# Kernel tuning notes

Hardware: AMD Instinct MI355X
Metric: run time of the kernel (lower is better)

Reference implementation:

```python
import jax, jax.numpy as jnp
import numpy as np

# MORR all-pass ring parameters (MORRConfig_20um defaults: attenuation / self-coupling)
A_MORR = 0.8578
R_MORR = 0.8578
KS = 3       # kernel_size
MB = 8       # miniblock (circulant block size)
BN_EPS = 1e-5


def mrr_roundtrip_phase_to_tr(phi):
    # through-port transmission of an all-pass microring vs roundtrip phase
    c = jnp.cos(phi)
    num = A_MORR * A_MORR - 2.0 * A_MORR * R_MORR * c + R_MORR * R_MORR
    den = 1.0 - 2.0 * A_MORR * R_MORR * c + (A_MORR * R_MORR) ** 2
    return num / den


def setup_inputs() -> dict:
    key = jax.random.key(0)
    k1, k2 = jax.random.split(key, 2)
    B, C, H, W = 64, 64, 32, 32
    outC = 64
    q = (C * KS * KS + MB - 1) // MB   # grid_dim_x = 72
    p = (outC + MB - 1) // MB          # grid_dim_y = 8
    x = jax.random.normal(k1, (B, C, H, W), jnp.float32)
    weight = jax.random.normal(k2, (p, q, MB), jnp.float32) * 0.05  # circulant eigen-vectors per block
    gamma = jnp.ones((outC,), jnp.float32)   # BatchNorm2d weight
    beta = jnp.zeros((outC,), jnp.float32)   # BatchNorm2d bias
    return {"x": x, "weight": weight, "gamma": gamma, "beta": beta}


def reference(x, weight, gamma, beta):
    B, C, H, W = x.shape
    p, q, mb = weight.shape
    outC = gamma.shape[0]
    Ho, Wo = H, W  # stride=1, padding=1, ks=3
    L = Ho * Wo
    # im2col (torch F.unfold ordering: C major, then kh, kw)
    xp = jnp.pad(x, ((0, 0), (0, 0), (1, 1), (1, 1)))
    cols = jnp.stack([xp[:, :, i:i + Ho, j:j + Wo]
                      for i in range(KS) for j in range(KS)], axis=2)  # [B,C,9,Ho,Wo]
    cols = cols.reshape(B, C * KS * KS, L).transpose(0, 2, 1)          # [B,L,C*k*k]
    assert C * KS * KS == q * mb, "patch dim must pad to q*mb"
    s = cols.reshape(B, L, q, mb)
    s = s * s  # optical intensity (power) fed into the MORR
    # block-circulant weight: Wc[p,q,i,j] = weight[p,q,(i-j) mod mb]
    i_idx = jnp.arange(mb)
    idx = (i_idx[:, None] - i_idx[None, :]) % mb
    Wc = weight[:, :, idx]                                             # [p,q,mb,mb]
    # accumulated roundtrip phase per output node
    phase = jnp.einsum('blqj,pqij->blpi', s, Wc)                       # [B,L,p,mb]
    tr = mrr_roundtrip_phase_to_tr(phase)
    out = tr.reshape(B, L, p * mb)[:, :, :outC]                        # truncate to out_channel
    out = out.transpose(0, 2, 1).reshape(B, outC, Ho, Wo)
    # BatchNorm2d (training mode: batch statistics) + Hardtanh(-1, 1)
    mean = out.mean(axis=(0, 2, 3), keepdims=True)
    var = out.var(axis=(0, 2, 3), keepdims=True)
    y = (out - mean) * jax.lax.rsqrt(var + BN_EPS)
    y = y * gamma[None, :, None, None] + beta[None, :, None, None]
    return jnp.clip(y, -1.0, 1.0)
```

## Files before the change

### kernel.cpp

```cpp
#include <hip/hip_runtime.h>


#define A_MORR 0.8578f
#define R_MORR 0.8578f
#define TR_C1 (A_MORR * A_MORR + R_MORR * R_MORR)
#define TR_C2 (-2.0f * A_MORR * R_MORR)
#define TR_C3 (1.0f + (A_MORR * R_MORR) * (A_MORR * R_MORR))
#define BN_EPS 1e-5f

#define NPIX 65536
#define X2_LO 26112
#define SMEM_BYTES 52224
#define NBLK 512

typedef __attribute__((ext_vector_type(8))) short bf16x8;
typedef __attribute__((ext_vector_type(16))) float f32x16;

__device__ __forceinline__ void bf16split(float s, unsigned short& h, unsigned short& l) {
    union { float f; unsigned u; } cv; cv.f = s;
    unsigned r = (cv.u + 0x7fffu + ((cv.u >> 16) & 1u)) & 0xffff0000u;
    h = (unsigned short)(r >> 16);
    union { unsigned u; float f; } hv; hv.u = r;
    float lo = s - hv.f;
    cv.f = lo;
    unsigned r2 = cv.u + 0x7fffu + ((cv.u >> 16) & 1u);
    l = (unsigned short)(r2 >> 16);
}

__global__ __launch_bounds__(256) void prep_kernel(const float* __restrict__ w,
                                                   char* __restrict__ wfrag) {
    int gtid = blockIdx.x * 256 + threadIdx.x;
    if (gtid < 36864) {
        int j    = gtid & 7;
        int lane = (gtid >> 3) & 63;
        int okm  = gtid >> 9;
        int mt   = okm & 1;
        int ks   = (okm >> 1) & 3;
        int off  = okm >> 3;
        int oc   = mt * 32 + (lane & 31);
        int c    = ks * 16 + (lane >> 5) * 8 + j;
        int kg   = c * 9 + off;
        float val = w[(oc >> 3) * 576 + (kg >> 3) * 8 + ((oc - kg) & 7)];
        unsigned short h, l;
        bf16split(val, h, l);
        ((unsigned short*)(wfrag + okm * 2048))[lane * 8 + j] = h;
        ((unsigned short*)(wfrag + okm * 2048 + 1024))[lane * 8 + j] = l;
    }
}

__global__ __launch_bounds__(512, 2) void conv_kernel(const float* __restrict__ x,
                                                      const char* __restrict__ wfrag,
                                                      float* __restrict__ out,
                                                      float* __restrict__ partials) {
    const int rt  = blockIdx.x;
    const int b   = blockIdx.y;
    const int bid = b * 8 + rt;
    const int tid = threadIdx.x;

    __shared__ __align__(16) char smem[SMEM_BYTES];

    if (tid < 192) {
        int prec = tid & 1;
        int g    = (tid >> 1) & 7;
        int rc   = tid >> 4;
        int r    = rc >> 1;
        int c    = (rc & 1) ? 33 : 0;
        *(uint4*)(smem + prec * X2_LO + ((r * 34 + c) << 7) + (g << 4)) = uint4{0, 0, 0, 0};
    }

    {
        const int rh  = tid & 1;
        const int co  = (tid >> 1) & 7;
        const int chp = tid >> 4;
        const float* xb = x + (size_t)(b * 64 + 2 * chp) * 1024;
#pragma unroll
        for (int r3 = 0; r3 < 3; ++r3) {
            int rr = rh * 3 + r3;
            int gr = rt * 4 - 1 + rr;
            float4 a0 = {0.f, 0.f, 0.f, 0.f}, a1 = {0.f, 0.f, 0.f, 0.f};
            if (gr >= 0 && gr < 32) {
                const float* rp = xb + gr * 32 + co * 4;
                a0 = *(const float4*)rp;
                a1 = *(const float4*)(rp + 1024);
            }
            float s0[4] = {a0.x * a0.x, a0.y * a0.y, a0.z * a0.z, a0.w * a0.w};
            float s1[4] = {a1.x * a1.x, a1.y * a1.y, a1.z * a1.z, a1.w * a1.w};
#pragma unroll
            for (int i = 0; i < 4; ++i) {
                unsigned short h0, l0, h1, l1;
                bf16split(s0[i], h0, l0);
                bf16split(s1[i], h1, l1);
                int c    = 1 + co * 4 + i;
                int base = ((rr * 34 + c) << 7) + (((chp >> 2) ^ (c & 7)) << 4)
                         + ((chp & 3) << 2);
                *(unsigned*)(smem + base)         = (unsigned)h0 | ((unsigned)h1 << 16);
                *(unsigned*)(smem + X2_LO + base) = (unsigned)l0 | ((unsigned)l1 << 16);
            }
        }
    }
    __syncthreads();

    const int lane = tid & 63;
    const int wv   = tid >> 6;
    const int wmt  = wv & 1;
    const int kh   = (wv >> 1) & 1;
    const int py   = wv >> 2;
    const int col  = lane & 31;
    const int hs   = lane >> 5;
    const int rowb = py * 2;

    f32x16 acc0, acc1;
#pragma unroll
    for (int i = 0; i < 16; ++i) { acc0[i] = 0.f; acc1[i] = 0.f; }

    const char* wbase = wfrag + wmt * 2048 + (size_t)lane * 16;

#pragma unroll
    for (int dj = 0; dj < 3; ++dj) {
        const int c  = col + dj;
        const int c7 = c & 7;
#pragma unroll
        for (int ksi = 0; ksi < 2; ++ksi) {
            const int ks = kh * 2 + ksi;
            const int g  = ((ks * 2 + hs) ^ c7) << 4;
            bf16x8 bh[4], bl[4];
#pragma unroll
            for (int rr = 0; rr < 4; ++rr) {
                const char* sp = smem + (((rowb + rr) * 34 + c) << 7) + g;
                bh[rr] = *(const bf16x8*)sp;
                bl[rr] = *(const bf16x8*)(sp + X2_LO);
            }
#pragma unroll
            for (int di = 0; di < 3; ++di) {
                const char* wp = wbase + (di * 3 + dj) * 16384 + ks * 4096;
                bf16x8 ah = *(const bf16x8*)wp;
                bf16x8 al = *(const bf16x8*)(wp + 1024);
                acc0 = __builtin_amdgcn_mfma_f32_32x32x16_bf16(ah, bh[di],     acc0, 0, 0, 0);
                acc1 = __builtin_amdgcn_mfma_f32_32x32x16_bf16(ah, bh[di + 1], acc1, 0, 0, 0);
                acc0 = __builtin_amdgcn_mfma_f32_32x32x16_bf16(ah, bl[di],     acc0, 0, 0, 0);
                acc1 = __builtin_amdgcn_mfma_f32_32x32x16_bf16(ah, bl[di + 1], acc1, 0, 0, 0);
                acc0 = __builtin_amdgcn_mfma_f32_32x32x16_bf16(al, bh[di],     acc0, 0, 0, 0);
                acc1 = __builtin_amdgcn_mfma_f32_32x32x16_bf16(al, bh[di + 1], acc1, 0, 0, 0);
            }
        }
    }

    float* mergef = (float*)smem;
    __syncthreads();
    {
        const int slot = (wmt * 2 + py) * 2;
        if (kh == 1) {
#pragma unroll
            for (int r = 0; r < 16; ++r) {
                mergef[((slot + 0) * 16 + r) * 64 + lane] = acc0[r];
                mergef[((slot + 1) * 16 + r) * 64 + lane] = acc1[r];
            }
        }
        __syncthreads();
        if (kh == 0) {
#pragma unroll
            for (int r = 0; r < 16; ++r) {
                float p0 = acc0[r] + mergef[((slot + 0) * 16 + r) * 64 + lane];
                float p1 = acc1[r] + mergef[((slot + 1) * 16 + r) * 64 + lane];
                float c0 = __cosf(p0);
                float c1 = __cosf(p1);
                acc0[r] = fmaf(TR_C2, c0, TR_C1) / fmaf(TR_C2, c0, TR_C3);
                acc1[r] = fmaf(TR_C2, c1, TR_C1) / fmaf(TR_C2, c1, TR_C3);
            }
        }
    }
    __syncthreads();

    float* red1 = mergef;
    float* red2 = red1 + 64 * 66;
    if (kh == 0) {
#pragma unroll
        for (int r = 0; r < 16; ++r) {
            int ocl  = (r & 3) + 8 * (r >> 2) + 4 * hs;
            float t0 = acc0[r], t1 = acc1[r];
            int ri = (wmt * 32 + ocl) * 66 + py * 32 + col;
            red1[ri] = t0 + t1;
            red2[ri] = t0 * t0 + t1 * t1;
        }
    }
    __syncthreads();
    if (tid < 64) {
        float s1 = 0.f, s2 = 0.f;
#pragma unroll
        for (int q = 0; q < 64; ++q) {
            s1 += red1[tid * 66 + q];
            s2 += red2[tid * 66 + q];
        }
        partials[(size_t)tid * NBLK + bid]        = s1;
        partials[(size_t)(64 + tid) * NBLK + bid] = s2;
    }

    if (kh == 0) {
        const size_t outbase = ((size_t)b * 64 + wmt * 32) * 1024 + rt * 128;
#pragma unroll
        for (int r = 0; r < 16; ++r) {
            int ocl  = (r & 3) + 8 * (r >> 2) + 4 * hs;
            size_t o = outbase + (size_t)ocl * 1024 + py * 64 + col;
            out[o]      = acc0[r];
            out[o + 32] = acc1[r];
        }
    }
}

__global__ __launch_bounds__(512) void stats_kernel(const float* __restrict__ partials,
                                                    const float* __restrict__ gamma,
                                                    const float* __restrict__ beta,
                                                    float* __restrict__ ss) {
    const int c   = blockIdx.x;
    const int tid = threadIdx.x;
    __shared__ float r1[512], r2[512];
    r1[tid] = partials[(size_t)c * NBLK + tid];
    r2[tid] = partials[(size_t)(64 + c) * NBLK + tid];
    __syncthreads();
#pragma unroll
    for (int s = 256; s > 0; s >>= 1) {
        if (tid < s) {
            r1[tid] += r1[tid + s];
            r2[tid] += r2[tid + s];
        }
        __syncthreads();
    }
    if (tid == 0) {
        const float invN = 1.0f / (float)NPIX;
        float mean = r1[0] * invN;
        float var  = r2[0] * invN - mean * mean;
        float sc   = gamma[c] * rsqrtf(var + BN_EPS);
        ss[c]      = sc;
        ss[64 + c] = beta[c] - mean * sc;
    }
}

__global__ __launch_bounds__(256) void norm_kernel(float* __restrict__ out,
                                                   const float* __restrict__ ss) {
    int i = blockIdx.x * 256 + threadIdx.x;
    float4 v = ((float4*)out)[i];
    int oc = (i >> 8) & 63;
    float sc = ss[oc];
    float sh = ss[64 + oc];
    v.x = fminf(1.0f, fmaxf(-1.0f, fmaf(v.x, sc, sh)));
    v.y = fminf(1.0f, fmaxf(-1.0f, fmaf(v.y, sc, sh)));
    v.z = fminf(1.0f, fmaxf(-1.0f, fmaf(v.z, sc, sh)));
    v.w = fminf(1.0f, fmaxf(-1.0f, fmaf(v.w, sc, sh)));
    ((float4*)out)[i] = v;
}

extern "C" void kernel_launch(void* const* d_in, const int* in_sizes, int n_in,
                              void* d_out, int out_size, void* d_ws, size_t ws_size,
                              hipStream_t stream) {
    const float* x     = (const float*)d_in[0];
    const float* w     = (const float*)d_in[1];
    const float* gamma = (const float*)d_in[2];
    const float* beta  = (const float*)d_in[3];
    float* out = (float*)d_out;

    char*  wfrag    = (char*)d_ws;
    float* partials = (float*)((char*)d_ws + 147456);
    float* ss       = partials + 128 * NBLK;

    hipLaunchKernelGGL(prep_kernel, dim3(144), dim3(256), 0, stream, w, wfrag);
    hipLaunchKernelGGL(conv_kernel, dim3(8, 64), dim3(512), 0, stream, x, wfrag, out, partials);
    hipLaunchKernelGGL(stats_kernel, dim3(64), dim3(512), 0, stream, partials, gamma, beta, ss);
    hipLaunchKernelGGL(norm_kernel, dim3(4096), dim3(256), 0, stream, out, ss);
}
```

Before: 42.00 us.

## Split K across four waves, register-cache weights, fuse epilogue with stats

Changes the wave decomposition from a 2x2 split over row pairs and K halves to a four-way K split, with each wave computing all four output rows. This lets each wave reuse B fragments across four accumulators, and the wave's nine weight fragments are preloaded into registers before the staging phase. Partial sums are merged through LDS in a chained sequence of five barriers. The transmission epilogue is fused with the output stores and the per-thread stat accumulation. Register pressure rises (four accumulators plus 18 weight vectors), and the serialized merge adds barriers and leaves only one wave in each M-tile half doing the epilogue.

After: 45.91 us. 9.3% more time.

```diff
diff --git a/kernel.cpp b/kernel.cpp
--- a/kernel.cpp
+++ b/kernel.cpp
@@ -57,7 +57,24 @@
     const int bid = b * 8 + rt;
     const int tid = threadIdx.x;
 
+    const int lane = tid & 63;
+    const int wv   = tid >> 6;
+    const int wmt  = wv & 1;
+    const int kq   = wv >> 1;
+    const int col  = lane & 31;
+    const int hs   = lane >> 5;
+
     __shared__ __align__(16) char smem[SMEM_BYTES];
+
+    bf16x8 wh[9], wl[9];
+    {
+        const char* wbase = wfrag + (size_t)wmt * 2048 + kq * 4096 + lane * 16;
+#pragma unroll
+        for (int t = 0; t < 9; ++t) {
+            wh[t] = *(const bf16x8*)(wbase + t * 16384);
+            wl[t] = *(const bf16x8*)(wbase + t * 16384 + 1024);
+        }
+    }
 
     if (tid < 192) {
         int prec = tid & 1;
@@ -100,110 +117,106 @@
     }
     __syncthreads();
 
-    const int lane = tid & 63;
-    const int wv   = tid >> 6;
-    const int wmt  = wv & 1;
-    const int kh   = (wv >> 1) & 1;
-    const int py   = wv >> 2;
-    const int col  = lane & 31;
-    const int hs   = lane >> 5;
-    const int rowb = py * 2;
-
-    f32x16 acc0, acc1;
-#pragma unroll
-    for (int i = 0; i < 16; ++i) { acc0[i] = 0.f; acc1[i] = 0.f; }
-
-    const char* wbase = wfrag + wmt * 2048 + (size_t)lane * 16;
+    f32x16 acc0, acc1, acc2, acc3;
+#pragma unroll
+    for (int i = 0; i < 16; ++i) { acc0[i] = 0.f; acc1[i] = 0.f; acc2[i] = 0.f; acc3[i] = 0.f; }
 
 #pragma unroll
     for (int dj = 0; dj < 3; ++dj) {
         const int c  = col + dj;
-        const int c7 = c & 7;
-#pragma unroll
-        for (int ksi = 0; ksi < 2; ++ksi) {
-            const int ks = kh * 2 + ksi;
-            const int g  = ((ks * 2 + hs) ^ c7) << 4;
-            bf16x8 bh[4], bl[4];
-#pragma unroll
-            for (int rr = 0; rr < 4; ++rr) {
-                const char* sp = smem + (((rowb + rr) * 34 + c) << 7) + g;
-                bh[rr] = *(const bf16x8*)sp;
-                bl[rr] = *(const bf16x8*)(sp + X2_LO);
-            }
-#pragma unroll
-            for (int di = 0; di < 3; ++di) {
-                const char* wp = wbase + (di * 3 + dj) * 16384 + ks * 4096;
-                bf16x8 ah = *(const bf16x8*)wp;
-                bf16x8 al = *(const bf16x8*)(wp + 1024);
-                acc0 = __builtin_amdgcn_mfma_f32_32x32x16_bf16(ah, bh[di],     acc0, 0, 0, 0);
-                acc1 = __builtin_amdgcn_mfma_f32_32x32x16_bf16(ah, bh[di + 1], acc1, 0, 0, 0);
-                acc0 = __builtin_amdgcn_mfma_f32_32x32x16_bf16(ah, bl[di],     acc0, 0, 0, 0);
-                acc1 = __builtin_amdgcn_mfma_f32_32x32x16_bf16(ah, bl[di + 1], acc1, 0, 0, 0);
-                acc0 = __builtin_amdgcn_mfma_f32_32x32x16_bf16(al, bh[di],     acc0, 0, 0, 0);
-                acc1 = __builtin_amdgcn_mfma_f32_32x32x16_bf16(al, bh[di + 1], acc1, 0, 0, 0);
-            }
-        }
-    }
-
-    float* mergef = (float*)smem;
-    __syncthreads();
-    {
-        const int slot = (wmt * 2 + py) * 2;
-        if (kh == 1) {
-#pragma unroll
-            for (int r = 0; r < 16; ++r) {
-                mergef[((slot + 0) * 16 + r) * 64 + lane] = acc0[r];
-                mergef[((slot + 1) * 16 + r) * 64 + lane] = acc1[r];
-            }
-        }
-        __syncthreads();
-        if (kh == 0) {
-#pragma unroll
-            for (int r = 0; r < 16; ++r) {
-                float p0 = acc0[r] + mergef[((slot + 0) * 16 + r) * 64 + lane];
-                float p1 = acc1[r] + mergef[((slot + 1) * 16 + r) * 64 + lane];
-                float c0 = __cosf(p0);
-                float c1 = __cosf(p1);
-                acc0[r] = fmaf(TR_C2, c0, TR_C1) / fmaf(TR_C2, c0, TR_C3);
-                acc1[r] = fmaf(TR_C2, c1, TR_C1) / fmaf(TR_C2, c1, TR_C3);
-            }
-        }
-    }
-    __syncthreads();
-
-    float* red1 = mergef;
-    float* red2 = red1 + 64 * 66;
-    if (kh == 0) {
-#pragma unroll
-        for (int r = 0; r < 16; ++r) {
-            int ocl  = (r & 3) + 8 * (r >> 2) + 4 * hs;
-            float t0 = acc0[r], t1 = acc1[r];
-            int ri = (wmt * 32 + ocl) * 66 + py * 32 + col;
-            red1[ri] = t0 + t1;
-            red2[ri] = t0 * t0 + t1 * t1;
+        const int g  = (((kq * 2 + hs) ^ (c & 7)) << 4);
+        bf16x8 bh[6], bl[6];
+#pragma unroll
+        for (int rr = 0; rr < 6; ++rr) {
+            const char* sp = smem + ((rr * 34 + c) << 7) + g;
+            bh[rr] = *(const bf16x8*)sp;
+            bl[rr] = *(const bf16x8*)(sp + X2_LO);
+        }
+#pragma unroll
+        for (int di = 0; di < 3; ++di) {
+            const bf16x8 ah = wh[di * 3 + dj];
+            const bf16x8 al = wl[di * 3 + dj];
+            acc0 = __builtin_amdgcn_mfma_f32_32x32x16_bf16(ah, bh[di + 0], acc0, 0, 0, 0);
+            acc1 = __builtin_amdgcn_mfma_f32_32x32x16_bf16(ah, bh[di + 1], acc1, 0, 0, 0);
+            acc2 = __builtin_amdgcn_mfma_f32_32x32x16_bf16(ah, bh[di + 2], acc2, 0, 0, 0);
+            acc3 = __builtin_amdgcn_mfma_f32_32x32x16_bf16(ah, bh[di + 3], acc3, 0, 0, 0);
+            acc0 = __builtin_amdgcn_mfma_f32_32x32x16_bf16(ah, bl[di + 0], acc0, 0, 0, 0);
+            acc1 = __builtin_amdgcn_mfma_f32_32x32x16_bf16(ah, bl[di + 1], acc1, 0, 0, 0);
+            acc2 = __builtin_amdgcn_mfma_f32_32x32x16_bf16(ah, bl[di + 2], acc2, 0, 0, 0);
+            acc3 = __builtin_amdgcn_mfma_f32_32x32x16_bf16(ah, bl[di + 3], acc3, 0, 0, 0);
+            acc0 = __builtin_amdgcn_mfma_f32_32x32x16_bf16(al, bh[di + 0], acc0, 0, 0, 0);
+            acc1 = __builtin_amdgcn_mfma_f32_32x32x16_bf16(al, bh[di + 1], acc1, 0, 0, 0);
+            acc2 = __builtin_amdgcn_mfma_f32_32x32x16_bf16(al, bh[di + 2], acc2, 0, 0, 0);
+            acc3 = __builtin_amdgcn_mfma_f32_32x32x16_bf16(al, bh[di + 3], acc3, 0, 0, 0);
+        }
+    }
+
+    float* mg = (float*)smem;
+#define SLOT_W() do {                                                          \
+    _Pragma("unroll") for (int j = 0; j < 16; ++j) {                           \
+        mg[((wmt * 4 + 0) * 16 + j) * 64 + lane] = acc0[j];                    \
+        mg[((wmt * 4 + 1) * 16 + j) * 64 + lane] = acc1[j];                    \
+        mg[((wmt * 4 + 2) * 16 + j) * 64 + lane] = acc2[j];                    \
+        mg[((wmt * 4 + 3) * 16 + j) * 64 + lane] = acc3[j];                    \
+    } } while (0)
+#define SLOT_A() do {                                                          \
+    _Pragma("unroll") for (int j = 0; j < 16; ++j) {                           \
+        acc0[j] += mg[((wmt * 4 + 0) * 16 + j) * 64 + lane];                   \
+        acc1[j] += mg[((wmt * 4 + 1) * 16 + j) * 64 + lane];                   \
+        acc2[j] += mg[((wmt * 4 + 2) * 16 + j) * 64 + lane];                   \
+        acc3[j] += mg[((wmt * 4 + 3) * 16 + j) * 64 + lane];                   \
+    } } while (0)
+
+    __syncthreads();
+    if (kq == 3) SLOT_W();
+    __syncthreads();
+    if (kq == 1) SLOT_A();
+    __syncthreads();
+    if (kq == 2) SLOT_W();
+    __syncthreads();
+    if (kq == 0) SLOT_A();
+    __syncthreads();
+    if (kq == 1) SLOT_W();
+    __syncthreads();
+
+    float* red1 = (float*)(smem + 32768);
+    float* red2 = red1 + 64 * 33;
+
+    if (kq == 0) {
+        SLOT_A();
+        float ts1[16], ts2[16];
+#pragma unroll
+        for (int j = 0; j < 16; ++j) { ts1[j] = 0.f; ts2[j] = 0.f; }
+        const size_t obase = ((size_t)b * 64 + wmt * 32) * 1024 + rt * 128;
+#define ROW_EPI(R, ACC) do {                                                   \
+    _Pragma("unroll") for (int j = 0; j < 16; ++j) {                           \
+        float cp = __cosf(ACC[j]);                                             \
+        float t  = fmaf(TR_C2, cp, TR_C1) / fmaf(TR_C2, cp, TR_C3);            \
+        int ocl  = (j & 3) + 8 * (j >> 2) + 4 * hs;                            \
+        out[obase + (size_t)ocl * 1024 + (R) * 32 + col] = t;                  \
+        ts1[j] += t; ts2[j] += t * t;                                          \
+    } } while (0)
+        ROW_EPI(0, acc0);
+        ROW_EPI(1, acc1);
+        ROW_EPI(2, acc2);
+        ROW_EPI(3, acc3);
+#pragma unroll
+        for (int j = 0; j < 16; ++j) {
+            int ocl = (j & 3) + 8 * (j >> 2) + 4 * hs;
+            red1[(wmt * 32 + ocl) * 33 + col] = ts1[j];
+            red2[(wmt * 32 + ocl) * 33 + col] = ts2[j];
         }
     }
     __syncthreads();
     if (tid < 64) {
         float s1 = 0.f, s2 = 0.f;
 #pragma unroll
-        for (int q = 0; q < 64; ++q) {
-            s1 += red1[tid * 66 + q];
-            s2 += red2[tid * 66 + q];
+        for (int q = 0; q < 32; ++q) {
+            s1 += red1[tid * 33 + q];
+            s2 += red2[tid * 33 + q];
         }
         partials[(size_t)tid * NBLK + bid]        = s1;
         partials[(size_t)(64 + tid) * NBLK + bid] = s2;
-    }
-
-    if (kh == 0) {
-        const size_t outbase = ((size_t)b * 64 + wmt * 32) * 1024 + rt * 128;
-#pragma unroll
-        for (int r = 0; r < 16; ++r) {
-            int ocl  = (r & 3) + 8 * (r >> 2) + 4 * hs;
-            size_t o = outbase + (size_t)ocl * 1024 + py * 64 + col;
-            out[o]      = acc0[r];
-            out[o + 32] = acc1[r];
-        }
     }
 }
 
```

## Halve conv block tile to two output rows, doubling grid and sharing transcendental work

Applied to the files above, without the earlier changes.

The conv kernel now processes 2 output rows per block with 256 threads instead of 4 rows with 512, doubling the grid to 1024 blocks and cutting shared memory to 34816 bytes. The k-split merge is rebalanced so both K-half waves each finalize one output row (cos/transfer and store), instead of only half the waves doing all epilogue work. Input staging is rewritten so each thread loads 8 channels for one column and writes 16-byte vectors. The workspace partials buffer grows to 1024 entries per channel, and the stats kernel sums two halves. The halo rows are now reloaded more often relative to useful rows, adding redundant input traffic.

Measured after the change: 41.24 us. Within noise of the previous version (-1.8%).

```diff
diff --git a/kernel.cpp b/kernel.cpp
--- a/kernel.cpp
+++ b/kernel.cpp
@@ -9,9 +9,9 @@
 #define BN_EPS 1e-5f
 
 #define NPIX 65536
-#define X2_LO 26112
-#define SMEM_BYTES 52224
-#define NBLK 512
+#define X2_LO 17408
+#define SMEM_BYTES 34816
+#define NBLK 1024
 
 typedef __attribute__((ext_vector_type(8))) short bf16x8;
 typedef __attribute__((ext_vector_type(16))) float f32x16;
@@ -48,66 +48,67 @@
     }
 }
 
-__global__ __launch_bounds__(512, 2) void conv_kernel(const float* __restrict__ x,
+__global__ __launch_bounds__(256, 4) void conv_kernel(const float* __restrict__ x,
                                                       const char* __restrict__ wfrag,
                                                       float* __restrict__ out,
                                                       float* __restrict__ partials) {
     const int rt  = blockIdx.x;
     const int b   = blockIdx.y;
-    const int bid = b * 8 + rt;
+    const int bid = b * 16 + rt;
     const int tid = threadIdx.x;
-
-    __shared__ __align__(16) char smem[SMEM_BYTES];
-
-    if (tid < 192) {
-        int prec = tid & 1;
-        int g    = (tid >> 1) & 7;
-        int rc   = tid >> 4;
-        int r    = rc >> 1;
-        int c    = (rc & 1) ? 33 : 0;
-        *(uint4*)(smem + prec * X2_LO + ((r * 34 + c) << 7) + (g << 4)) = uint4{0, 0, 0, 0};
-    }
-
-    {
-        const int rh  = tid & 1;
-        const int co  = (tid >> 1) & 7;
-        const int chp = tid >> 4;
-        const float* xb = x + (size_t)(b * 64 + 2 * chp) * 1024;
-#pragma unroll
-        for (int r3 = 0; r3 < 3; ++r3) {
-            int rr = rh * 3 + r3;
-            int gr = rt * 4 - 1 + rr;
-            float4 a0 = {0.f, 0.f, 0.f, 0.f}, a1 = {0.f, 0.f, 0.f, 0.f};
-            if (gr >= 0 && gr < 32) {
-                const float* rp = xb + gr * 32 + co * 4;
-                a0 = *(const float4*)rp;
-                a1 = *(const float4*)(rp + 1024);
-            }
-            float s0[4] = {a0.x * a0.x, a0.y * a0.y, a0.z * a0.z, a0.w * a0.w};
-            float s1[4] = {a1.x * a1.x, a1.y * a1.y, a1.z * a1.z, a1.w * a1.w};
-#pragma unroll
-            for (int i = 0; i < 4; ++i) {
-                unsigned short h0, l0, h1, l1;
-                bf16split(s0[i], h0, l0);
-                bf16split(s1[i], h1, l1);
-                int c    = 1 + co * 4 + i;
-                int base = ((rr * 34 + c) << 7) + (((chp >> 2) ^ (c & 7)) << 4)
-                         + ((chp & 3) << 2);
-                *(unsigned*)(smem + base)         = (unsigned)h0 | ((unsigned)h1 << 16);
-                *(unsigned*)(smem + X2_LO + base) = (unsigned)l0 | ((unsigned)l1 << 16);
-            }
-        }
-    }
-    __syncthreads();
 
     const int lane = tid & 63;
     const int wv   = tid >> 6;
     const int wmt  = wv & 1;
-    const int kh   = (wv >> 1) & 1;
-    const int py   = wv >> 2;
+    const int kh   = wv >> 1;
     const int col  = lane & 31;
     const int hs   = lane >> 5;
-    const int rowb = py * 2;
+
+    __shared__ __align__(16) char smem[SMEM_BYTES];
+
+    if (tid < 128) {
+        int pr = tid & 1;
+        int q  = (tid >> 1) & 7;
+        int rc = tid >> 4;
+        int r  = rc >> 1;
+        int cc = (rc & 1) ? 33 : 0;
+        int g  = q ^ (cc & 7);
+        *(uint4*)(smem + pr * X2_LO + ((r * 34 + cc) << 7) + (g << 4)) = uint4{0, 0, 0, 0};
+    }
+
+    {
+        const int co = tid & 31;
+        const int qg = tid >> 5;
+        const int c  = 1 + co;
+        const int gw = (qg ^ (c & 7)) << 4;
+        const float* xb = x + (size_t)(b * 64 + qg * 8) * 1024 + co;
+#pragma unroll
+        for (int r = 0; r < 4; ++r) {
+            int gr = rt * 2 - 1 + r;
+            float v[8];
+#pragma unroll
+            for (int j = 0; j < 8; ++j) v[j] = 0.0f;
+            if (gr >= 0 && gr < 32) {
+#pragma unroll
+                for (int j = 0; j < 8; ++j) v[j] = xb[j * 1024 + gr * 32];
+            }
+            unsigned hp[4], lp[4];
+#pragma unroll
+            for (int p = 0; p < 4; ++p) {
+                unsigned short h0, l0, h1, l1;
+                float s0 = v[2 * p] * v[2 * p];
+                float s1 = v[2 * p + 1] * v[2 * p + 1];
+                bf16split(s0, h0, l0);
+                bf16split(s1, h1, l1);
+                hp[p] = (unsigned)h0 | ((unsigned)h1 << 16);
+                lp[p] = (unsigned)l0 | ((unsigned)l1 << 16);
+            }
+            char* dst = smem + ((r * 34 + c) << 7) + gw;
+            *(uint4*)dst            = uint4{hp[0], hp[1], hp[2], hp[3]};
+            *(uint4*)(dst + X2_LO)  = uint4{lp[0], lp[1], lp[2], lp[3]};
+        }
+    }
+    __syncthreads();
 
     f32x16 acc0, acc1;
 #pragma unroll
@@ -117,16 +118,16 @@
 
 #pragma unroll
     for (int dj = 0; dj < 3; ++dj) {
-        const int c  = col + dj;
-        const int c7 = c & 7;
+        const int c2 = col + dj;
+        const int c7 = c2 & 7;
 #pragma unroll
         for (int ksi = 0; ksi < 2; ++ksi) {
             const int ks = kh * 2 + ksi;
-            const int g  = ((ks * 2 + hs) ^ c7) << 4;
+            const int gg = ((ks * 2 + hs) ^ c7) << 4;
             bf16x8 bh[4], bl[4];
 #pragma unroll
             for (int rr = 0; rr < 4; ++rr) {
-                const char* sp = smem + (((rowb + rr) * 34 + c) << 7) + g;
+                const char* sp = smem + ((rr * 34 + c2) << 7) + gg;
                 bh[rr] = *(const bf16x8*)sp;
                 bl[rr] = *(const bf16x8*)(sp + X2_LO);
             }
@@ -145,65 +146,65 @@
         }
     }
 
-    float* mergef = (float*)smem;
-    __syncthreads();
-    {
-        const int slot = (wmt * 2 + py) * 2;
-        if (kh == 1) {
-#pragma unroll
-            for (int r = 0; r < 16; ++r) {
-                mergef[((slot + 0) * 16 + r) * 64 + lane] = acc0[r];
-                mergef[((slot + 1) * 16 + r) * 64 + lane] = acc1[r];
-            }
-        }
-        __syncthreads();
+    float* mg = (float*)smem;
+    __syncthreads();
+    {
+        const int wslot = wmt * 2 + kh;
         if (kh == 0) {
 #pragma unroll
-            for (int r = 0; r < 16; ++r) {
-                float p0 = acc0[r] + mergef[((slot + 0) * 16 + r) * 64 + lane];
-                float p1 = acc1[r] + mergef[((slot + 1) * 16 + r) * 64 + lane];
-                float c0 = __cosf(p0);
-                float c1 = __cosf(p1);
-                acc0[r] = fmaf(TR_C2, c0, TR_C1) / fmaf(TR_C2, c0, TR_C3);
-                acc1[r] = fmaf(TR_C2, c1, TR_C1) / fmaf(TR_C2, c1, TR_C3);
-            }
-        }
-    }
-    __syncthreads();
-
-    float* red1 = mergef;
+            for (int j = 0; j < 16; ++j) mg[(wslot * 16 + j) * 64 + lane] = acc1[j];
+        } else {
+#pragma unroll
+            for (int j = 0; j < 16; ++j) mg[(wslot * 16 + j) * 64 + lane] = acc0[j];
+        }
+    }
+    __syncthreads();
+    f32x16 phi;
+    {
+        const int rslot = wmt * 2 + (kh ^ 1);
+        if (kh == 0) {
+#pragma unroll
+            for (int j = 0; j < 16; ++j) phi[j] = acc0[j] + mg[(rslot * 16 + j) * 64 + lane];
+        } else {
+#pragma unroll
+            for (int j = 0; j < 16; ++j) phi[j] = acc1[j] + mg[(rslot * 16 + j) * 64 + lane];
+        }
+    }
+
+    float tv[16];
+    {
+        const size_t obase = ((size_t)b * 64 + wmt * 32) * 1024 + (rt * 2 + kh) * 32 + col;
+#pragma unroll
+        for (int j = 0; j < 16; ++j) {
+            float cp = __cosf(phi[j]);
+            float t  = fmaf(TR_C2, cp, TR_C1) / fmaf(TR_C2, cp, TR_C3);
+            tv[j] = t;
+            int ocl = (j & 3) + 8 * (j >> 2) + 4 * hs;
+            out[obase + (size_t)ocl * 1024] = t;
+        }
+    }
+
+    float* red1 = (float*)smem;
     float* red2 = red1 + 64 * 66;
-    if (kh == 0) {
-#pragma unroll
-        for (int r = 0; r < 16; ++r) {
-            int ocl  = (r & 3) + 8 * (r >> 2) + 4 * hs;
-            float t0 = acc0[r], t1 = acc1[r];
-            int ri = (wmt * 32 + ocl) * 66 + py * 32 + col;
-            red1[ri] = t0 + t1;
-            red2[ri] = t0 * t0 + t1 * t1;
-        }
+    __syncthreads();
+#pragma unroll
+    for (int j = 0; j < 16; ++j) {
+        int ocl = (j & 3) + 8 * (j >> 2) + 4 * hs;
+        int ri  = (wmt * 32 + ocl) * 66 + kh * 33 + col;
+        red1[ri] = tv[j];
+        red2[ri] = tv[j] * tv[j];
     }
     __syncthreads();
     if (tid < 64) {
         float s1 = 0.f, s2 = 0.f;
 #pragma unroll
-        for (int q = 0; q < 64; ++q) {
-            s1 += red1[tid * 66 + q];
-            s2 += red2[tid * 66 + q];
+        for (int k = 0; k < 64; ++k) {
+            int idx = tid * 66 + (k >> 5) * 33 + (k & 31);
+            s1 += red1[idx];
+            s2 += red2[idx];
         }
         partials[(size_t)tid * NBLK + bid]        = s1;
         partials[(size_t)(64 + tid) * NBLK + bid] = s2;
-    }
-
-    if (kh == 0) {
-        const size_t outbase = ((size_t)b * 64 + wmt * 32) * 1024 + rt * 128;
-#pragma unroll
-        for (int r = 0; r < 16; ++r) {
-            int ocl  = (r & 3) + 8 * (r >> 2) + 4 * hs;
-            size_t o = outbase + (size_t)ocl * 1024 + py * 64 + col;
-            out[o]      = acc0[r];
-            out[o + 32] = acc1[r];
-        }
     }
 }
 
@@ -214,8 +215,9 @@
     const int c   = blockIdx.x;
     const int tid = threadIdx.x;
     __shared__ float r1[512], r2[512];
-    r1[tid] = partials[(size_t)c * NBLK + tid];
-    r2[tid] = partials[(size_t)(64 + c) * NBLK + tid];
+    r1[tid] = partials[(size_t)c * NBLK + tid] + partials[(size_t)c * NBLK + 512 + tid];
+    r2[tid] = partials[(size_t)(64 + c) * NBLK + tid]
+            + partials[(size_t)(64 + c) * NBLK + 512 + tid];
     __syncthreads();
 #pragma unroll
     for (int s = 256; s > 0; s >>= 1) {
@@ -263,7 +265,7 @@
     float* ss       = partials + 128 * NBLK;
 
     hipLaunchKernelGGL(prep_kernel, dim3(144), dim3(256), 0, stream, w, wfrag);
-    hipLaunchKernelGGL(conv_kernel, dim3(8, 64), dim3(512), 0, stream, x, wfrag, out, partials);
+    hipLaunchKernelGGL(conv_kernel, dim3(16, 64), dim3(256), 0, stream, x, wfrag, out, partials);
     hipLaunchKernelGGL(stats_kernel, dim3(64), dim3(512), 0, stream, partials, gamma, beta, ss);
     hipLaunchKernelGGL(norm_kernel, dim3(4096), dim3(256), 0, stream, out, ss);
 }
```
